# Kernel optimization log

Measured on AMD Instinct MI355X. Metric: run time of the kernel, lower is better.

Reference implementation:

```python
import jax, jax.numpy as jnp
import numpy as np

B, L, D, H = 2, 2048, 1024, 16
HD = D // H  # 64


def rotate_half(x):
    x1, x2 = x[..., : x.shape[-1] // 2], x[..., x.shape[-1] // 2 :]
    return jnp.concatenate([-x2, x1], axis=-1)


def apply_rope(x, cos, sin):
    # x: (B, H, L, HD); cos/sin: (1, L, HD)
    c = cos[:, None, : x.shape[2], :]
    s = sin[:, None, : x.shape[2], :]
    return x * c + rotate_half(x) * s


def setup_inputs() -> dict:
    key = jax.random.key(0)
    ks = jax.random.split(key, 16)
    query = jax.random.normal(ks[0], (B, L, D), jnp.float32)
    k_in = jax.random.normal(ks[1], (B, L, D), jnp.float32)
    v_in = jax.random.normal(ks[2], (B, L, D), jnp.float32)
    key_padding_mask = jax.random.uniform(ks[3], (B, L)) < 0.2
    # genuine RoPE tables
    inv_freq = 1.0 / (10000.0 ** (jnp.arange(0, HD, 2, dtype=jnp.float32) / HD))
    ang = jnp.arange(L, dtype=jnp.float32)[:, None] * inv_freq[None, :]  # (L, HD/2)
    ang = jnp.concatenate([ang, ang], axis=-1)  # (L, HD)
    rope_cos = jnp.cos(ang)[None]  # (1, L, HD)
    rope_sin = jnp.sin(ang)[None]
    scale = 0.02
    Wq = jax.random.normal(ks[4], (D, D), jnp.float32) * scale
    bq = jnp.zeros((D,), jnp.float32)
    Wk = jax.random.normal(ks[5], (D, D), jnp.float32) * scale
    bk = jnp.zeros((D,), jnp.float32)
    Wv = jax.random.normal(ks[6], (D, D), jnp.float32) * scale
    bv = jnp.zeros((D,), jnp.float32)
    Wg = jax.random.normal(ks[7], (D, D), jnp.float32) * scale  # init zeros in torch; random for grad coverage
    bg = jnp.ones((D,), jnp.float32)
    Wo = jax.random.normal(ks[8], (D, D), jnp.float32) * scale
    bo = jnp.zeros((D,), jnp.float32)
    return dict(query=query, key=k_in, value=v_in, key_padding_mask=key_padding_mask,
                rope_cos=rope_cos, rope_sin=rope_sin,
                Wq=Wq, bq=bq, Wk=Wk, bk=bk, Wv=Wv, bv=bv,
                Wg=Wg, bg=bg, Wo=Wo, bo=bo)


def reference(query, key, value, key_padding_mask, rope_cos, rope_sin,
              Wq, bq, Wk, bk, Wv, bv, Wg, bg, Wo, bo):
    Bq, Lq, _ = query.shape
    Lk = key.shape[1]
    # torch Linear: x @ W.T + b
    Q = (query @ Wq.T + bq).reshape(Bq, Lq, H, HD).transpose(0, 2, 1, 3)
    K = (key @ Wk.T + bk).reshape(Bq, Lk, H, HD).transpose(0, 2, 1, 3)
    V = (value @ Wv.T + bv).reshape(Bq, Lk, H, HD).transpose(0, 2, 1, 3)
    K = apply_rope(K, rope_cos, rope_sin)
    Q = apply_rope(Q, rope_cos, rope_sin)
    scale = 1.0 / jnp.sqrt(jnp.asarray(HD, query.dtype))
    scores = jnp.einsum('bhqd,bhkd->bhqk', Q, K) * scale
    allow = ~key_padding_mask[:, None, None, :]  # (B,1,1,Lk): True = attend
    scores = jnp.where(allow, scores, -jnp.inf)
    attn = jax.nn.softmax(scores, axis=-1)
    out = jnp.einsum('bhqk,bhkd->bhqd', attn, V)
    out = jnp.nan_to_num(out, nan=0.0)
    out = out.transpose(0, 2, 1, 3).reshape(Bq, Lq, D)
    gate = jax.nn.sigmoid(query @ Wg.T + bg)
    out = out * gate
    out = out @ Wo.T + bo
    return out
```

## Files before the change

### kernel.cpp

```cpp
#include <hip/hip_runtime.h>
#include <hip/hip_bf16.h>
#include <cstdint>


constexpr int NB = 2, NL = 2048, ND = 1024, NH = 16, NHD = 64;
constexpr int NM = NB * NL;

typedef __bf16 bf16_t;
typedef __bf16 bf16x8 __attribute__((ext_vector_type(8)));
typedef __bf16 bf16x4 __attribute__((ext_vector_type(4)));
typedef float f32x4 __attribute__((ext_vector_type(4)));
typedef float f32x16 __attribute__((ext_vector_type(16)));
typedef unsigned int uint2v __attribute__((ext_vector_type(2)));

typedef const __attribute__((address_space(1))) void* gas_ptr;
typedef __attribute__((address_space(3))) void* las_ptr;

__device__ __forceinline__ void async_load16(const void* g, void* l) {
  __builtin_amdgcn_global_load_lds((gas_ptr)g, (las_ptr)l, 16, 0, 0);
}

__device__ __forceinline__ unsigned cvtpk_bf16(float lo, float hi) {
  unsigned r;
  asm("v_cvt_pk_bf16_f32 %0, %1, %2" : "=v"(r) : "v"(lo), "v"(hi));
  return r;
}

__device__ __forceinline__ void pl32_swap(unsigned& a, unsigned& b) {
#if __has_builtin(__builtin_amdgcn_permlane32_swap)
  uint2v r = __builtin_amdgcn_permlane32_swap(a, b, false, false);
  a = r.x; b = r.y;
#else
  asm volatile("v_permlane32_swap_b32 %0, %1" : "+v"(a), "+v"(b));
#endif
}

struct CvtArgs {
  const float* s[8];
  bf16_t* d[8];
};
__global__ __launch_bounds__(256) void cvt8_kernel(CvtArgs a) {
  int y = blockIdx.y;
  int n4 = (y < 3) ? (NM * ND / 4) : (ND * ND / 4);
  const float* src = a.s[y];
  bf16_t* dst = a.d[y];
  for (int i = blockIdx.x * 256 + threadIdx.x; i < n4; i += gridDim.x * 256) {
    float4 v = ((const float4*)src)[i];
    bf16x4 o;
    o[0] = (bf16_t)v.x; o[1] = (bf16_t)v.y; o[2] = (bf16_t)v.z; o[3] = (bf16_t)v.w;
    ((bf16x4*)dst)[i] = o;
  }
}

template <int MODE>
__global__ __launch_bounds__(256) void gemm_kernel(
    const bf16_t* __restrict__ Aq, const bf16_t* __restrict__ Ak, const bf16_t* __restrict__ Av,
    const bf16_t* __restrict__ W0, const bf16_t* __restrict__ W1,
    const bf16_t* __restrict__ W2, const bf16_t* __restrict__ W3,
    const float* __restrict__ b0, const float* __restrict__ b1,
    const float* __restrict__ b2, const float* __restrict__ b3,
    const float* __restrict__ ctab, const float* __restrict__ stab,
    bf16_t* __restrict__ Qr, bf16_t* __restrict__ Kr, bf16_t* __restrict__ Vt,
    float* __restrict__ Gp, float* __restrict__ Out) {
  __shared__ __align__(16) bf16_t lA[2][128 * 64];
  __shared__ __align__(16) bf16_t lB[2][128 * 64];
  const int tid = threadIdx.x, lane = tid & 63, w = tid >> 6;
  const int wm = w >> 1, wn = w & 1;
  const int lr = lane & 15, lg = lane >> 4;

  const int lin = blockIdx.x;
  const int xcd = lin & 7, idx = lin >> 3;
  constexpr int G = (MODE == 1) ? 4 : 1;
  const int ntile = xcd * G + (idx & (G - 1));
  const int mtile = idx / G;

  const bf16_t* Asrc;
  const bf16_t* Wsrc;
  int nofs, t = 0;
  if constexpr (MODE == 1) {
    t = ntile >> 3;
    Asrc = (t == 1) ? Ak : (t == 2) ? Av : Aq;
    Wsrc = (t == 0) ? W0 : (t == 1) ? W1 : (t == 2) ? W2 : W3;
    nofs = (ntile & 7) * 128;
  } else {
    Asrc = Aq; Wsrc = W0; nofs = ntile * 128;
  }
  const bf16_t* Ablk = Asrc + mtile * 128 * ND;
  const bf16_t* Wblk = Wsrc + nofs * ND;

  f32x4 acc[4][4];
#pragma unroll
  for (int i = 0; i < 4; ++i)
#pragma unroll
    for (int j = 0; j < 4; ++j)
#pragma unroll
      for (int k = 0; k < 4; ++k) acc[i][j][k] = 0.f;

  auto STAGE = [&](int b, int kb) {
#pragma unroll
    for (int p = 0; p < 4; ++p) {
      int q = w * 256 + p * 64 + lane;
      int r = q >> 3, c = q & 7;
      int cs = c ^ (r & 7);
      async_load16(Ablk + r * ND + kb * 64 + cs * 8, &lA[b][(w * 256 + p * 64) * 8]);
      async_load16(Wblk + r * ND + kb * 64 + cs * 8, &lB[b][(w * 256 + p * 64) * 8]);
    }
  };
  auto COMPUTE = [&](int b) {
    const bf16_t* pA = lA[b];
    const bf16_t* pB = lB[b];
#pragma unroll
    for (int ks = 0; ks < 2; ++ks) {
      bf16x8 af[4], bfr[4];
#pragma unroll
      for (int i = 0; i < 4; ++i) {
        int ra = wm * 64 + i * 16 + lr;
        int ca = (ks * 4 + lg) ^ (ra & 7);
        af[i] = *(const bf16x8*)(pA + ra * 64 + ca * 8);
        int rb = wn * 64 + i * 16 + lr;
        int cb = (ks * 4 + lg) ^ (rb & 7);
        bfr[i] = *(const bf16x8*)(pB + rb * 64 + cb * 8);
      }
#pragma unroll
      for (int i = 0; i < 4; ++i)
#pragma unroll
        for (int j = 0; j < 4; ++j)
          acc[i][j] = __builtin_amdgcn_mfma_f32_16x16x32_bf16(af[i], bfr[j], acc[i][j], 0, 0, 0);
    }
  };

  STAGE(0, 0);
  __syncthreads();
  int buf = 0;
  for (int kb = 0; kb < 15; ++kb) {
    STAGE(buf ^ 1, kb + 1);
    COMPUTE(buf);
    __syncthreads();
    buf ^= 1;
  }
  COMPUTE(buf);

  if constexpr (MODE == 0) {
#pragma unroll
    for (int j = 0; j < 4; ++j) {
      int nn = ntile * 128 + wn * 64 + j * 16 + lr;
      float bias = b0[nn];
#pragma unroll
      for (int i = 0; i < 4; ++i)
#pragma unroll
        for (int rg = 0; rg < 4; ++rg) {
          int mm = mtile * 128 + wm * 64 + i * 16 + lg * 4 + rg;
          Out[mm * ND + nn] = acc[i][j][rg] + bias;
        }
    }
  } else {
    const int fbase = nofs + wn * 64;
    const int h = fbase >> 6;
    if (t < 2) {
      bf16_t* dst = (t == 0) ? Qr : Kr;
      const float* bias = (t == 0) ? b0 : b1;
      const float qs = (t == 0) ? 0.18033688011112042f : 1.0f;
#pragma unroll
      for (int i = 0; i < 4; ++i)
#pragma unroll
        for (int rg = 0; rg < 4; ++rg) {
          int mm = mtile * 128 + wm * 64 + i * 16 + lg * 4 + rg;
          int bb = mm >> 11, l = mm & (NL - 1);
          bf16_t* rowp = dst + ((bb * NH + h) * NL + l) * NHD;
          const float* crow = ctab + l * NHD;
          const float* srow = stab + l * NHD;
#pragma unroll
          for (int j = 0; j < 2; ++j) {
            int dlo = j * 16 + lr, dhi = dlo + 32;
            float xlo = acc[i][j][rg] + bias[fbase + dlo];
            float xhi = acc[i][j + 2][rg] + bias[fbase + dhi];
            float olo = (xlo * crow[dlo] - xhi * srow[dlo]) * qs;
            float ohi = (xhi * crow[dhi] + xlo * srow[dhi]) * qs;
            rowp[dlo] = (bf16_t)olo;
            rowp[dhi] = (bf16_t)ohi;
          }
        }
    } else if (t == 2) {
#pragma unroll
      for (int i = 0; i < 4; ++i) {
        int mmb = mtile * 128 + wm * 64 + i * 16 + lg * 4;
        int bb = mmb >> 11, l0 = mmb & (NL - 1);
#pragma unroll
        for (int j = 0; j < 4; ++j) {
          int d = j * 16 + lr;
          float bias = b2[fbase + d];
          unsigned u01 = cvtpk_bf16(acc[i][j][0] + bias, acc[i][j][1] + bias);
          unsigned u23 = cvtpk_bf16(acc[i][j][2] + bias, acc[i][j][3] + bias);
          unsigned long long pk = (unsigned long long)u01 | ((unsigned long long)u23 << 32);
          *(unsigned long long*)(Vt + ((bb * NH + h) * NHD + d) * NL + l0) = pk;
        }
      }
    } else {
#pragma unroll
      for (int i = 0; i < 4; ++i)
#pragma unroll
        for (int rg = 0; rg < 4; ++rg) {
          int mm = mtile * 128 + wm * 64 + i * 16 + lg * 4 + rg;
#pragma unroll
          for (int j = 0; j < 4; ++j) {
            int f = fbase + j * 16 + lr;
            Gp[mm * ND + f] = acc[i][j][rg] + b3[f];
          }
        }
    }
  }
}

__global__ __launch_bounds__(256) void attn_kernel(
    const bf16_t* __restrict__ Qr, const bf16_t* __restrict__ Kr, const bf16_t* __restrict__ Vt,
    const int* __restrict__ mask, const float* __restrict__ Gp, bf16_t* __restrict__ X) {
  __shared__ __align__(16) bf16_t lK[2][64 * 64];
  __shared__ __align__(16) bf16_t lV[2][64 * 64];

  int lin = blockIdx.y * gridDim.x + blockIdx.x;
  int swz = (lin & 7) * 64 + (lin >> 3);
  const int qb = swz & 15, bh = swz >> 4;
  const int bb = bh >> 4, h = bh & 15;

  const int tid = threadIdx.x, lane = tid & 63, w = tid >> 6;
  const int ql = lane & 31, hi = lane >> 5;

  const bf16_t* Kbh = Kr + bh * NL * NHD;
  const bf16_t* Vbh = Vt + bh * NHD * NL;
  const int q = qb * 128 + w * 32 + ql;

  const bf16_t* Qp = Qr + (bh * NL + q) * NHD + 8 * hi;
  bf16x8 qf[4];
#pragma unroll
  for (int c = 0; c < 4; ++c) qf[c] = *(const bf16x8*)(Qp + 16 * c);
  bf16x8 qf5 = {};
  qf5[0] = (bf16_t)(hi ? 0.f : 1.f);

  f32x16 acc[2];
#pragma unroll
  for (int dt = 0; dt < 2; ++dt)
#pragma unroll
    for (int r = 0; r < 16; ++r) acc[dt][r] = 0.f;
  float lrun = 0.f;

#pragma unroll
  for (int p2 = 0; p2 < 2; ++p2) {
    int u = p2 * 256 + tid;
    int r = u >> 3, c = u & 7, cs = c ^ (r & 7);
    async_load16(Kbh + r * NHD + cs * 8, &lK[0][u * 8]);
    async_load16(Vbh + r * NL + cs * 8, &lV[0][u * 8]);
  }
  int curmv = mask[bb * NL + lane];
  __syncthreads();

  int buf = 0;
  for (int t = 0; t < NL / 64; ++t) {
    int nextmv = 0;
    if (t + 1 < NL / 64) {
      int kb1 = (t + 1) * 64;
#pragma unroll
      for (int p2 = 0; p2 < 2; ++p2) {
        int u = p2 * 256 + tid;
        int r = u >> 3, c = u & 7, cs = c ^ (r & 7);
        async_load16(Kbh + (kb1 + r) * NHD + cs * 8, &lK[buf ^ 1][u * 8]);
        async_load16(Vbh + r * NL + kb1 + cs * 8, &lV[buf ^ 1][u * 8]);
      }
      nextmv = mask[bb * NL + kb1 + lane];
    }

    unsigned long long bm = __ballot(curmv != 0);
    unsigned bmw0 = (unsigned)bm, bmw1 = (unsigned)(bm >> 32);
    const bf16_t* lKb = lK[buf];
    const bf16_t* lVb = lV[buf];

    float bv0 = ((bmw0 >> ql) & 1u) ? -1008.f : -8.f;
    float bv1 = ((bmw1 >> ql) & 1u) ? -1008.f : -8.f;
    bf16x8 kf5a = {}, kf5b = {};
    kf5a[0] = (bf16_t)(hi ? 0.f : bv0);
    kf5b[0] = (bf16_t)(hi ? 0.f : bv1);

    f32x16 st[2];
    __builtin_amdgcn_s_setprio(1);
#pragma unroll
    for (int t2 = 0; t2 < 2; ++t2) {
      int row = 32 * t2 + ql;
      const bf16_t* kbase = lKb + row * 64;
      f32x16 s;
#pragma unroll
      for (int r = 0; r < 16; ++r) s[r] = 0.f;
#pragma unroll
      for (int c = 0; c < 4; ++c) {
        int un = (2 * c + hi) ^ (row & 7);
        bf16x8 kf = *(const bf16x8*)(kbase + un * 8);
        s = __builtin_amdgcn_mfma_f32_32x32x16_bf16(kf, qf[c], s, 0, 0, 0);
      }
      s = __builtin_amdgcn_mfma_f32_32x32x16_bf16(t2 ? kf5b : kf5a, qf5, s, 0, 0, 0);
      st[t2] = s;
    }
    __builtin_amdgcn_s_setprio(0);

#pragma unroll
    for (int t2 = 0; t2 < 2; ++t2)
#pragma unroll
      for (int r = 0; r < 16; ++r) st[t2][r] = exp2f(st[t2][r]);
    float ts[16];
#pragma unroll
    for (int r = 0; r < 16; ++r) ts[r] = st[0][r] + st[1][r];
#pragma unroll
    for (int off = 8; off > 0; off >>= 1)
#pragma unroll
      for (int r = 0; r < 8; ++r)
        if (r < off) ts[r] += ts[r + off];
    lrun += ts[0];

    unsigned wds[2][4][2];
#pragma unroll
    for (int t2 = 0; t2 < 2; ++t2)
#pragma unroll
      for (int r1 = 0; r1 < 4; ++r1) {
        wds[t2][r1][0] = cvtpk_bf16(st[t2][4 * r1 + 0], st[t2][4 * r1 + 1]);
        wds[t2][r1][1] = cvtpk_bf16(st[t2][4 * r1 + 2], st[t2][4 * r1 + 3]);
      }
    bf16x8 pf[4];
#pragma unroll
    for (int kc = 0; kc < 4; ++kc) {
      int t2 = kc >> 1, r1a = 2 * (kc & 1);
      unsigned a0 = wds[t2][r1a][0], b0 = wds[t2][r1a + 1][0];
      unsigned a1 = wds[t2][r1a][1], b1 = wds[t2][r1a + 1][1];
      pl32_swap(a0, b0);
      pl32_swap(a1, b1);
      union { unsigned u[4]; bf16x8 v; } uu;
      uu.u[0] = a0; uu.u[1] = a1; uu.u[2] = b0; uu.u[3] = b1;
      pf[kc] = uu.v;
    }

    __builtin_amdgcn_s_setprio(1);
#pragma unroll
    for (int dt = 0; dt < 2; ++dt) {
      int row = 32 * dt + ql;
      const bf16_t* vbase = lVb + row * 64;
      f32x16 a = acc[dt];
#pragma unroll
      for (int kc = 0; kc < 4; ++kc) {
        int un = (2 * kc + hi) ^ (row & 7);
        bf16x8 vf = *(const bf16x8*)(vbase + un * 8);
        a = __builtin_amdgcn_mfma_f32_32x32x16_bf16(vf, pf[kc], a, 0, 0, 0);
      }
      acc[dt] = a;
    }
    __builtin_amdgcn_s_setprio(0);

    __syncthreads();
    curmv = nextmv;
    buf ^= 1;
  }

  float lt = lrun + __shfl_xor(lrun, 32, 64);
  float rinv = lt > 0.f ? 1.f / lt : 0.f;
  const int rowbase = (bb * NL + q) * ND + h * NHD;
#pragma unroll
  for (int dt = 0; dt < 2; ++dt)
#pragma unroll
    for (int r1 = 0; r1 < 4; ++r1) {
      int dbase = 32 * dt + 8 * r1 + 4 * hi;
      float4 g4 = *(const float4*)(Gp + rowbase + dbase);
      float gg[4] = {g4.x, g4.y, g4.z, g4.w};
      bf16x4 o;
#pragma unroll
      for (int j = 0; j < 4; ++j) {
        float gate = 1.f / (1.f + exp2f(-1.44269504f * gg[j]));
        o[j] = (bf16_t)(acc[dt][4 * r1 + j] * rinv * gate);
      }
      *(bf16x4*)(X + rowbase + dbase) = o;
    }
}

extern "C" void kernel_launch(void* const* d_in, const int* in_sizes, int n_in,
                              void* d_out, int out_size, void* d_ws, size_t ws_size,
                              hipStream_t stream) {
  const float* query = (const float*)d_in[0];
  const float* key   = (const float*)d_in[1];
  const float* value = (const float*)d_in[2];
  const int*   maskp = (const int*)d_in[3];
  const float* rcos  = (const float*)d_in[4];
  const float* rsin  = (const float*)d_in[5];
  const float* Wq = (const float*)d_in[6];  const float* bq = (const float*)d_in[7];
  const float* Wk = (const float*)d_in[8];  const float* bk = (const float*)d_in[9];
  const float* Wv = (const float*)d_in[10]; const float* bv = (const float*)d_in[11];
  const float* Wg = (const float*)d_in[12]; const float* bg = (const float*)d_in[13];
  const float* Wo = (const float*)d_in[14]; const float* bo = (const float*)d_in[15];

  constexpr size_t MB = 1ull << 20;
  char* ws = (char*)d_ws;
  bf16_t* qbb = (bf16_t*)(ws + 0 * MB);
  bf16_t* kbb = (bf16_t*)(ws + 8 * MB);
  bf16_t* vbb = (bf16_t*)(ws + 16 * MB);
  bf16_t* wqb = (bf16_t*)(ws + 24 * MB);
  bf16_t* wkb = (bf16_t*)(ws + 26 * MB);
  bf16_t* wvb = (bf16_t*)(ws + 28 * MB);
  bf16_t* wgb = (bf16_t*)(ws + 30 * MB);
  bf16_t* wob = (bf16_t*)(ws + 32 * MB);
  bf16_t* Qr  = (bf16_t*)(ws + 34 * MB);
  bf16_t* Kr  = (bf16_t*)(ws + 42 * MB);
  bf16_t* Vt  = (bf16_t*)(ws + 50 * MB);
  float*  Gp  = (float*)(ws + 58 * MB);
  bf16_t* Xb  = (bf16_t*)(ws + 74 * MB);

  CvtArgs ca;
  ca.s[0] = query; ca.d[0] = qbb;
  ca.s[1] = key;   ca.d[1] = kbb;
  ca.s[2] = value; ca.d[2] = vbb;
  ca.s[3] = Wq;    ca.d[3] = wqb;
  ca.s[4] = Wk;    ca.d[4] = wkb;
  ca.s[5] = Wv;    ca.d[5] = wvb;
  ca.s[6] = Wg;    ca.d[6] = wgb;
  ca.s[7] = Wo;    ca.d[7] = wob;
  cvt8_kernel<<<dim3(1024, 8), 256, 0, stream>>>(ca);

  gemm_kernel<1><<<1024, 256, 0, stream>>>(
      qbb, kbb, vbb, wqb, wkb, wvb, wgb, bq, bk, bv, bg, rcos, rsin,
      Qr, Kr, Vt, Gp, nullptr);

  attn_kernel<<<dim3(16, 32), 256, 0, stream>>>(Qr, Kr, Vt, maskp, Gp, Xb);

  gemm_kernel<0><<<256, 256, 0, stream>>>(
      Xb, nullptr, nullptr, wob, nullptr, nullptr, nullptr,
      bo, nullptr, nullptr, nullptr, nullptr, nullptr,
      nullptr, nullptr, nullptr, nullptr, (float*)d_out);
}
```

Baseline: 159.5 us.

## Use 128-key attention tiles with precomputed LDS offsets and store gate in bf16

The attention kernel now stages 128 keys per iteration instead of 64, in two 64-key halves per barrier. Global source pointers and LDS read offsets are precomputed, and the loop is unrolled by two so buffer indices are constant. This halves the barriers and loop overhead per key and doubles LDS use. The gate pre-activation is also written and read as bf16 instead of fp32, which cuts that tensor's memory traffic at some precision cost.

```diff
diff --git a/kernel.cpp b/kernel.cpp
--- a/kernel.cpp
+++ b/kernel.cpp
@@ -61,7 +61,7 @@
     const float* __restrict__ b2, const float* __restrict__ b3,
     const float* __restrict__ ctab, const float* __restrict__ stab,
     bf16_t* __restrict__ Qr, bf16_t* __restrict__ Kr, bf16_t* __restrict__ Vt,
-    float* __restrict__ Gp, float* __restrict__ Out) {
+    bf16_t* __restrict__ Gb, float* __restrict__ Out) {
   __shared__ __align__(16) bf16_t lA[2][128 * 64];
   __shared__ __align__(16) bf16_t lB[2][128 * 64];
   const int tid = threadIdx.x, lane = tid & 63, w = tid >> 6;
@@ -204,7 +204,7 @@
 #pragma unroll
           for (int j = 0; j < 4; ++j) {
             int f = fbase + j * 16 + lr;
-            Gp[mm * ND + f] = acc[i][j][rg] + b3[f];
+            Gb[mm * ND + f] = (bf16_t)(acc[i][j][rg] + b3[f]);
           }
         }
     }
@@ -213,9 +213,9 @@
 
 __global__ __launch_bounds__(256) void attn_kernel(
     const bf16_t* __restrict__ Qr, const bf16_t* __restrict__ Kr, const bf16_t* __restrict__ Vt,
-    const int* __restrict__ mask, const float* __restrict__ Gp, bf16_t* __restrict__ X) {
-  __shared__ __align__(16) bf16_t lK[2][64 * 64];
-  __shared__ __align__(16) bf16_t lV[2][64 * 64];
+    const int* __restrict__ mask, const bf16_t* __restrict__ Gb, bf16_t* __restrict__ X) {
+  __shared__ __align__(16) bf16_t lK[2][128 * 64];
+  __shared__ __align__(16) bf16_t lV[2][64 * 128];
 
   int lin = blockIdx.y * gridDim.x + blockIdx.x;
   int swz = (lin & 7) * 64 + (lin >> 3);
@@ -243,116 +243,146 @@
     for (int r = 0; r < 16; ++r) acc[dt][r] = 0.f;
   float lrun = 0.f;
 
-#pragma unroll
-  for (int p2 = 0; p2 < 2; ++p2) {
-    int u = p2 * 256 + tid;
-    int r = u >> 3, c = u & 7, cs = c ^ (r & 7);
-    async_load16(Kbh + r * NHD + cs * 8, &lK[0][u * 8]);
-    async_load16(Vbh + r * NL + cs * 8, &lV[0][u * 8]);
-  }
-  int curmv = mask[bb * NL + lane];
+  const bf16_t* gsrc[8];
+#pragma unroll
+  for (int j = 0; j < 8; ++j) {
+    if (j < 4) {
+      int u = j * 256 + tid;
+      int r = u >> 3, c = u & 7, cs = c ^ (r & 7);
+      gsrc[j] = Kbh + r * NHD + cs * 8;
+    } else {
+      int v = (j - 4) * 256 + tid;
+      int r = v >> 4, c = v & 15, cs = (c & 8) | ((c & 7) ^ (r & 7));
+      gsrc[j] = Vbh + r * NL + cs * 8;
+    }
+  }
+  auto STAGE = [&](int b) {
+#pragma unroll
+    for (int j = 0; j < 8; ++j) {
+      if (j < 4) {
+        async_load16(gsrc[j], &lK[b][(j * 256 + tid) * 8]);
+        gsrc[j] += 128 * NHD;
+      } else {
+        async_load16(gsrc[j], &lV[b][((j - 4) * 256 + tid) * 8]);
+        gsrc[j] += 128;
+      }
+    }
+  };
+
+  unsigned rdK[2][4], rdV[2][4];
+#pragma unroll
+  for (int t2 = 0; t2 < 2; ++t2)
+#pragma unroll
+    for (int c = 0; c < 4; ++c) {
+      unsigned un = ((2 * c + hi) ^ (ql & 7)) * 16;
+      rdK[t2][c] = (32 * t2 + ql) * 128 + un;
+      rdV[t2][c] = (32 * t2 + ql) * 256 + un;
+    }
+  const char* lKc = (const char*)lK;
+  const char* lVc = (const char*)lV;
+
+  STAGE(0);
+  int mv0 = mask[bb * NL + lane];
+  int mv1 = mask[bb * NL + 64 + lane];
   __syncthreads();
 
-  int buf = 0;
-  for (int t = 0; t < NL / 64; ++t) {
-    int nextmv = 0;
-    if (t + 1 < NL / 64) {
-      int kb1 = (t + 1) * 64;
-#pragma unroll
-      for (int p2 = 0; p2 < 2; ++p2) {
-        int u = p2 * 256 + tid;
-        int r = u >> 3, c = u & 7, cs = c ^ (r & 7);
-        async_load16(Kbh + (kb1 + r) * NHD + cs * 8, &lK[buf ^ 1][u * 8]);
-        async_load16(Vbh + r * NL + kb1 + cs * 8, &lV[buf ^ 1][u * 8]);
-      }
-      nextmv = mask[bb * NL + kb1 + lane];
-    }
-
-    unsigned long long bm = __ballot(curmv != 0);
-    unsigned bmw0 = (unsigned)bm, bmw1 = (unsigned)(bm >> 32);
-    const bf16_t* lKb = lK[buf];
-    const bf16_t* lVb = lV[buf];
-
-    float bv0 = ((bmw0 >> ql) & 1u) ? -1008.f : -8.f;
-    float bv1 = ((bmw1 >> ql) & 1u) ? -1008.f : -8.f;
-    bf16x8 kf5a = {}, kf5b = {};
-    kf5a[0] = (bf16_t)(hi ? 0.f : bv0);
-    kf5b[0] = (bf16_t)(hi ? 0.f : bv1);
-
-    f32x16 st[2];
-    __builtin_amdgcn_s_setprio(1);
-#pragma unroll
-    for (int t2 = 0; t2 < 2; ++t2) {
-      int row = 32 * t2 + ql;
-      const bf16_t* kbase = lKb + row * 64;
-      f32x16 s;
-#pragma unroll
-      for (int r = 0; r < 16; ++r) s[r] = 0.f;
-#pragma unroll
-      for (int c = 0; c < 4; ++c) {
-        int un = (2 * c + hi) ^ (row & 7);
-        bf16x8 kf = *(const bf16x8*)(kbase + un * 8);
-        s = __builtin_amdgcn_mfma_f32_32x32x16_bf16(kf, qf[c], s, 0, 0, 0);
-      }
-      s = __builtin_amdgcn_mfma_f32_32x32x16_bf16(t2 ? kf5b : kf5a, qf5, s, 0, 0, 0);
-      st[t2] = s;
-    }
-    __builtin_amdgcn_s_setprio(0);
-
-#pragma unroll
-    for (int t2 = 0; t2 < 2; ++t2)
-#pragma unroll
-      for (int r = 0; r < 16; ++r) st[t2][r] = exp2f(st[t2][r]);
+  auto BODY = [&](int buf, int t) {
+    int nmv0 = 0, nmv1 = 0;
+    if (t < 15) {
+      STAGE(buf ^ 1);
+      nmv0 = mask[bb * NL + (t + 1) * 128 + lane];
+      nmv1 = mask[bb * NL + (t + 1) * 128 + 64 + lane];
+    }
+    unsigned long long bmA = __ballot(mv0 != 0);
+    unsigned long long bmB = __ballot(mv1 != 0);
+    unsigned mws[4] = {(unsigned)bmA, (unsigned)(bmA >> 32),
+                       (unsigned)bmB, (unsigned)(bmB >> 32)};
+    bf16x8 kf5[4];
+#pragma unroll
+    for (int g = 0; g < 4; ++g) {
+      float bv = ((mws[g] >> ql) & 1u) ? -1008.f : -8.f;
+      bf16x8 z = {};
+      z[0] = (bf16_t)(hi ? 0.f : bv);
+      kf5[g] = z;
+    }
     float ts[16];
 #pragma unroll
-    for (int r = 0; r < 16; ++r) ts[r] = st[0][r] + st[1][r];
+    for (int hh = 0; hh < 2; ++hh) {
+      f32x16 st[2];
+      __builtin_amdgcn_s_setprio(1);
+#pragma unroll
+      for (int t2 = 0; t2 < 2; ++t2) {
+        f32x16 s;
+#pragma unroll
+        for (int r = 0; r < 16; ++r) s[r] = 0.f;
+#pragma unroll
+        for (int c = 0; c < 4; ++c) {
+          bf16x8 kf = *(const bf16x8*)(lKc + rdK[t2][c] + buf * 16384 + hh * 8192);
+          s = __builtin_amdgcn_mfma_f32_32x32x16_bf16(kf, qf[c], s, 0, 0, 0);
+        }
+        s = __builtin_amdgcn_mfma_f32_32x32x16_bf16(kf5[hh * 2 + t2], qf5, s, 0, 0, 0);
+        st[t2] = s;
+      }
+      __builtin_amdgcn_s_setprio(0);
+
+#pragma unroll
+      for (int t2 = 0; t2 < 2; ++t2)
+#pragma unroll
+        for (int r = 0; r < 16; ++r) st[t2][r] = exp2f(st[t2][r]);
+#pragma unroll
+      for (int r = 0; r < 16; ++r) {
+        float v = st[0][r] + st[1][r];
+        if (hh == 0) ts[r] = v; else ts[r] += v;
+      }
+
+      unsigned wds[2][4][2];
+#pragma unroll
+      for (int t2 = 0; t2 < 2; ++t2)
+#pragma unroll
+        for (int r1 = 0; r1 < 4; ++r1) {
+          wds[t2][r1][0] = cvtpk_bf16(st[t2][4 * r1 + 0], st[t2][4 * r1 + 1]);
+          wds[t2][r1][1] = cvtpk_bf16(st[t2][4 * r1 + 2], st[t2][4 * r1 + 3]);
+        }
+      bf16x8 pf[4];
+#pragma unroll
+      for (int kc = 0; kc < 4; ++kc) {
+        int t2 = kc >> 1, r1a = 2 * (kc & 1);
+        unsigned a0 = wds[t2][r1a][0], b0 = wds[t2][r1a + 1][0];
+        unsigned a1 = wds[t2][r1a][1], b1 = wds[t2][r1a + 1][1];
+        pl32_swap(a0, b0);
+        pl32_swap(a1, b1);
+        union { unsigned u[4]; bf16x8 v; } uu;
+        uu.u[0] = a0; uu.u[1] = a1; uu.u[2] = b0; uu.u[3] = b1;
+        pf[kc] = uu.v;
+      }
+
+      __builtin_amdgcn_s_setprio(1);
+#pragma unroll
+      for (int dt = 0; dt < 2; ++dt) {
+        f32x16 a = acc[dt];
+#pragma unroll
+        for (int kc = 0; kc < 4; ++kc) {
+          bf16x8 vf = *(const bf16x8*)(lVc + rdV[dt][kc] + buf * 16384 + hh * 128);
+          a = __builtin_amdgcn_mfma_f32_32x32x16_bf16(vf, pf[kc], a, 0, 0, 0);
+        }
+        acc[dt] = a;
+      }
+      __builtin_amdgcn_s_setprio(0);
+    }
 #pragma unroll
     for (int off = 8; off > 0; off >>= 1)
 #pragma unroll
       for (int r = 0; r < 8; ++r)
         if (r < off) ts[r] += ts[r + off];
     lrun += ts[0];
-
-    unsigned wds[2][4][2];
-#pragma unroll
-    for (int t2 = 0; t2 < 2; ++t2)
-#pragma unroll
-      for (int r1 = 0; r1 < 4; ++r1) {
-        wds[t2][r1][0] = cvtpk_bf16(st[t2][4 * r1 + 0], st[t2][4 * r1 + 1]);
-        wds[t2][r1][1] = cvtpk_bf16(st[t2][4 * r1 + 2], st[t2][4 * r1 + 3]);
-      }
-    bf16x8 pf[4];
-#pragma unroll
-    for (int kc = 0; kc < 4; ++kc) {
-      int t2 = kc >> 1, r1a = 2 * (kc & 1);
-      unsigned a0 = wds[t2][r1a][0], b0 = wds[t2][r1a + 1][0];
-      unsigned a1 = wds[t2][r1a][1], b1 = wds[t2][r1a + 1][1];
-      pl32_swap(a0, b0);
-      pl32_swap(a1, b1);
-      union { unsigned u[4]; bf16x8 v; } uu;
-      uu.u[0] = a0; uu.u[1] = a1; uu.u[2] = b0; uu.u[3] = b1;
-      pf[kc] = uu.v;
-    }
-
-    __builtin_amdgcn_s_setprio(1);
-#pragma unroll
-    for (int dt = 0; dt < 2; ++dt) {
-      int row = 32 * dt + ql;
-      const bf16_t* vbase = lVb + row * 64;
-      f32x16 a = acc[dt];
-#pragma unroll
-      for (int kc = 0; kc < 4; ++kc) {
-        int un = (2 * kc + hi) ^ (row & 7);
-        bf16x8 vf = *(const bf16x8*)(vbase + un * 8);
-        a = __builtin_amdgcn_mfma_f32_32x32x16_bf16(vf, pf[kc], a, 0, 0, 0);
-      }
-      acc[dt] = a;
-    }
-    __builtin_amdgcn_s_setprio(0);
-
     __syncthreads();
-    curmv = nextmv;
-    buf ^= 1;
+    mv0 = nmv0;
+    mv1 = nmv1;
+  };
+
+  for (int tt = 0; tt < 8; ++tt) {
+    BODY(0, 2 * tt);
+    BODY(1, 2 * tt + 1);
   }
 
   float lt = lrun + __shfl_xor(lrun, 32, 64);
@@ -363,12 +393,11 @@
 #pragma unroll
     for (int r1 = 0; r1 < 4; ++r1) {
       int dbase = 32 * dt + 8 * r1 + 4 * hi;
-      float4 g4 = *(const float4*)(Gp + rowbase + dbase);
-      float gg[4] = {g4.x, g4.y, g4.z, g4.w};
+      bf16x4 g4 = *(const bf16x4*)(Gb + rowbase + dbase);
       bf16x4 o;
 #pragma unroll
       for (int j = 0; j < 4; ++j) {
-        float gate = 1.f / (1.f + exp2f(-1.44269504f * gg[j]));
+        float gate = 1.f / (1.f + exp2f(-1.44269504f * (float)g4[j]));
         o[j] = (bf16_t)(acc[dt][4 * r1 + j] * rinv * gate);
       }
       *(bf16x4*)(X + rowbase + dbase) = o;
@@ -403,7 +432,7 @@
   bf16_t* Qr  = (bf16_t*)(ws + 34 * MB);
   bf16_t* Kr  = (bf16_t*)(ws + 42 * MB);
   bf16_t* Vt  = (bf16_t*)(ws + 50 * MB);
-  float*  Gp  = (float*)(ws + 58 * MB);
+  bf16_t* Gb  = (bf16_t*)(ws + 58 * MB);
   bf16_t* Xb  = (bf16_t*)(ws + 74 * MB);
 
   CvtArgs ca;
@@ -419,9 +448,9 @@
 
   gemm_kernel<1><<<1024, 256, 0, stream>>>(
       qbb, kbb, vbb, wqb, wkb, wvb, wgb, bq, bk, bv, bg, rcos, rsin,
-      Qr, Kr, Vt, Gp, nullptr);
-
-  attn_kernel<<<dim3(16, 32), 256, 0, stream>>>(Qr, Kr, Vt, maskp, Gp, Xb);
+      Qr, Kr, Vt, Gb, nullptr);
+
+  attn_kernel<<<dim3(16, 32), 256, 0, stream>>>(Qr, Kr, Vt, maskp, Gb, Xb);
 
   gemm_kernel<0><<<256, 256, 0, stream>>>(
       Xb, nullptr, nullptr, wob, nullptr, nullptr, nullptr,
```

After: 152.8 us. 1.04x faster.
